# Performance work log

Hardware: AMD Instinct MI355X
Metric: run time of the kernel (lower is better)

Reference implementation:

```python
import jax, jax.numpy as jnp
import numpy as np

K = 3
IN_C, OUT_C = 64, 64
B, N, E = 2, 50000, 800000


def setup_inputs() -> dict:
    key = jax.random.key(0)
    k1, k2, k3, k4, k5 = jax.random.split(key, 5)
    x = jax.random.normal(k1, (B, N, IN_C), dtype=jnp.float32)
    edge_index = jax.random.randint(k2, (2, E), 0, N, dtype=jnp.int64)
    edge_weight = jax.random.uniform(k3, (E,), dtype=jnp.float32)
    stdv = 1.0 / np.sqrt(IN_C * K)
    weight = jax.random.uniform(k4, (K, IN_C, OUT_C), dtype=jnp.float32, minval=-stdv, maxval=stdv)
    bias = jax.random.uniform(k5, (OUT_C,), dtype=jnp.float32, minval=-stdv, maxval=stdv)
    return {"x": x, "edge_index": edge_index, "edge_weight": edge_weight, "weight": weight, "bias": bias}


def reference(x, edge_index, edge_weight, weight, bias):
    row, col = edge_index[0], edge_index[1]
    num_nodes = x.shape[1]
    # remove self loops (mask them out; equivalent math)
    keep = (row != col)
    ew = jnp.where(keep, edge_weight, 0.0)
    # degree counts edges per source node (ones), excluding self loops
    deg = jax.ops.segment_sum(keep.astype(x.dtype), row, num_segments=num_nodes)
    deg_inv_sqrt = jnp.where(deg > 0, deg ** -0.5, 0.0)
    lap = -deg_inv_sqrt[row] * ew * deg_inv_sqrt[col]  # [E]

    def spmm(m):
        # m: [B, N, C] -> gather cols, scale by lap, scatter-add to rows
        vals = m[:, col, :] * lap[None, :, None]        # [B, E, C]
        return jnp.zeros_like(m).at[:, row, :].add(vals)

    Tx0 = x
    out = jnp.matmul(Tx0, weight[0])
    Tx1 = spmm(Tx0)
    out = out + jnp.matmul(Tx1, weight[1])
    for k in range(2, weight.shape[0]):
        Tx2 = 2.0 * spmm(Tx1) - Tx0
        out = out + jnp.matmul(Tx2, weight[k])
        Tx0, Tx1 = Tx1, Tx2
    return out + bias
```

## Files before the change

kernel.cpp:

```cpp
#include <hip/hip_runtime.h>

#define N_NODES 50000
#define N_EDGES 800000
#define N_B 2
#define N_C 64
#define BN_ROWS (N_B * N_NODES)

__device__ inline unsigned short f2bf(float f) {
  unsigned int u = __float_as_uint(f);
  return (unsigned short)((u + 0x7fffu + ((u >> 16) & 1u)) >> 16);
}
__device__ inline float bf2f(unsigned short h) { return __uint_as_float(((unsigned int)h) << 16); }
__device__ inline float lof(unsigned int u) { return __uint_as_float(u << 16); }
__device__ inline float hif(unsigned int u) { return __uint_as_float(u & 0xffff0000u); }

__global__ __launch_bounds__(256) void k_deg(const int* __restrict__ ei, int* __restrict__ deg) {
  int e = blockIdx.x * 256 + threadIdx.x;
  if (e >= N_EDGES) return;
  int r = ei[e];
  int c = ei[N_EDGES + e];
  if (r != c) atomicAdd(&deg[r], 1);
}

__global__ __launch_bounds__(256) void k_offsets(const int* __restrict__ deg, int* __restrict__ counter,
                                                 int* __restrict__ rowptr, int* __restrict__ cursor,
                                                 float* __restrict__ dis) {
  int n = blockIdx.x * 256 + threadIdx.x;
  int lane = threadIdx.x & 63;
  int d = (n < N_NODES) ? deg[n] : 0;
  int pre = d;
#pragma unroll
  for (int off = 1; off < 64; off <<= 1) {
    int v = __shfl_up(pre, off);
    if (lane >= off) pre += v;
  }
  int waveTotal = __shfl(pre, 63);
  int wbase = 0;
  if (lane == 63) wbase = atomicAdd(counter, waveTotal);
  wbase = __shfl(wbase, 63);
  if (n < N_NODES) {
    int off0 = wbase + pre - d;
    rowptr[n] = off0;
    cursor[n] = off0;
    dis[n] = d > 0 ? rsqrtf((float)d) : 0.0f;
  }
}

__global__ __launch_bounds__(256) void k_fill(const int* __restrict__ ei, const float* __restrict__ ew,
                                              const float* __restrict__ dis, int* __restrict__ cursor,
                                              int2* __restrict__ ccv) {
  int e = blockIdx.x * 256 + threadIdx.x;
  if (e >= N_EDGES) return;
  int r = ei[e];
  int c = ei[N_EDGES + e];
  if (r == c) return;
  float v = -dis[r] * ew[e] * dis[c];
  int pos = atomicAdd(&cursor[r], 1);
  ccv[pos] = make_int2(c, __float_as_int(v));
}

__global__ __launch_bounds__(256) void k_cvt(const float* __restrict__ x, unsigned short* __restrict__ xb) {
  int i = blockIdx.x * 256 + threadIdx.x;
  if (i >= BN_ROWS * 16) return;
  float4 v = ((const float4*)x)[i];
  ushort4 h;
  h.x = f2bf(v.x); h.y = f2bf(v.y); h.z = f2bf(v.z); h.w = f2bf(v.w);
  ((ushort4*)xb)[i] = h;
}

#define UNPK_FMA(Q, A0, A1, A2, A3, A4, A5, A6, A7, V) \
  A0 += (V) * lof(Q.x); A1 += (V) * hif(Q.x); \
  A2 += (V) * lof(Q.y); A3 += (V) * hif(Q.y); \
  A4 += (V) * lof(Q.z); A5 += (V) * hif(Q.z); \
  A6 += (V) * lof(Q.w); A7 += (V) * hif(Q.w);

#define RED3(A) { A += __shfl_xor(A, 8); A += __shfl_xor(A, 16); A += __shfl_xor(A, 32); }

template <int BFOUT>
__global__ __launch_bounds__(256) void k_spmm(const unsigned short* __restrict__ src, void* __restrict__ dstv,
                                              const int* __restrict__ rowptr, const int* __restrict__ deg,
                                              const int2* __restrict__ ccv) {
  int n = (blockIdx.x * 256 + threadIdx.x) >> 6;
  int lane = threadIdx.x & 63;
  if (n >= N_NODES) return;
  const int g = lane >> 3;
  const int cg = lane & 7;
  const unsigned short* s0 = src;
  const unsigned short* s1 = src + (size_t)N_NODES * N_C;
  int r0 = rowptr[n];
  int end = r0 + deg[n];
  float a00 = 0, a01 = 0, a02 = 0, a03 = 0, a04 = 0, a05 = 0, a06 = 0, a07 = 0;
  float a10 = 0, a11 = 0, a12 = 0, a13 = 0, a14 = 0, a15 = 0, a16 = 0, a17 = 0;
#pragma unroll 2
  for (int i = r0; i < end; i += 8) {
    int idx = i + g;
    bool ok = idx < end;
    int2 pe = ccv[ok ? idx : (end - 1)];
    float val = ok ? __int_as_float(pe.y) : 0.0f;
    size_t off = (size_t)pe.x * N_C + cg * 8;
    uint4 q0 = *(const uint4*)(s0 + off);
    uint4 q1 = *(const uint4*)(s1 + off);
    UNPK_FMA(q0, a00, a01, a02, a03, a04, a05, a06, a07, val)
    UNPK_FMA(q1, a10, a11, a12, a13, a14, a15, a16, a17, val)
  }
  RED3(a00) RED3(a01) RED3(a02) RED3(a03) RED3(a04) RED3(a05) RED3(a06) RED3(a07)
  RED3(a10) RED3(a11) RED3(a12) RED3(a13) RED3(a14) RED3(a15) RED3(a16) RED3(a17)
  if (BFOUT) {
    unsigned short* d = (unsigned short*)dstv;
    if (g == 0) {
      uint4 o;
      o.x = (unsigned)f2bf(a00) | ((unsigned)f2bf(a01) << 16);
      o.y = (unsigned)f2bf(a02) | ((unsigned)f2bf(a03) << 16);
      o.z = (unsigned)f2bf(a04) | ((unsigned)f2bf(a05) << 16);
      o.w = (unsigned)f2bf(a06) | ((unsigned)f2bf(a07) << 16);
      *(uint4*)(d + (size_t)n * N_C + cg * 8) = o;
    } else if (g == 1) {
      uint4 o;
      o.x = (unsigned)f2bf(a10) | ((unsigned)f2bf(a11) << 16);
      o.y = (unsigned)f2bf(a12) | ((unsigned)f2bf(a13) << 16);
      o.z = (unsigned)f2bf(a14) | ((unsigned)f2bf(a15) << 16);
      o.w = (unsigned)f2bf(a16) | ((unsigned)f2bf(a17) << 16);
      *(uint4*)(d + ((size_t)N_NODES + n) * N_C + cg * 8) = o;
    }
  } else {
    float* d = (float*)dstv;
    if (g == 0) {
      *(float4*)(d + (size_t)n * N_C + cg * 8) = make_float4(a00, a01, a02, a03);
      *(float4*)(d + (size_t)n * N_C + cg * 8 + 4) = make_float4(a04, a05, a06, a07);
    } else if (g == 1) {
      *(float4*)(d + ((size_t)N_NODES + n) * N_C + cg * 8) = make_float4(a10, a11, a12, a13);
      *(float4*)(d + ((size_t)N_NODES + n) * N_C + cg * 8 + 4) = make_float4(a14, a15, a16, a17);
    }
  }
}

#define FMA4(ACC, AV, WV) \
  ACC.x += (AV) * (WV).x; ACC.y += (AV) * (WV).y; ACC.z += (AV) * (WV).z; ACC.w += (AV) * (WV).w;

#define CH_STEP(Wb, KK, A0, A1, A2, A3) { \
  const float4 wv0 = *(const float4*)&(Wb)[(k4 + (KK)) * 64 + tx8]; \
  const float4 wv1 = *(const float4*)&(Wb)[(k4 + (KK)) * 64 + tx8 + 4]; \
  FMA4(acc00, A0, wv0) FMA4(acc01, A0, wv1) \
  FMA4(acc10, A1, wv0) FMA4(acc11, A1, wv1) \
  FMA4(acc20, A2, wv0) FMA4(acc21, A2, wv1) \
  FMA4(acc30, A3, wv0) FMA4(acc31, A3, wv1) }

#define CH_BODY(A0, A1, A2, A3, Wb) \
    CH_STEP(Wb, 0, A0.x, A1.x, A2.x, A3.x) \
    CH_STEP(Wb, 1, A0.y, A1.y, A2.y, A3.y) \
    CH_STEP(Wb, 2, A0.z, A1.z, A2.z, A3.z) \
    CH_STEP(Wb, 3, A0.w, A1.w, A2.w, A3.w)

#define CH_PASS_F32(Ab, Wb) \
  _Pragma("unroll 2") \
  for (int k4 = 0; k4 < 64; k4 += 4) { \
    const float4 a0 = *(const float4*)&(Ab)[r0 * 64 + (size_t)k4]; \
    const float4 a1 = *(const float4*)&(Ab)[r1 * 64 + (size_t)k4]; \
    const float4 a2 = *(const float4*)&(Ab)[r2 * 64 + (size_t)k4]; \
    const float4 a3 = *(const float4*)&(Ab)[r3 * 64 + (size_t)k4]; \
    CH_BODY(a0, a1, a2, a3, Wb) \
  }

__device__ inline float4 u4f(ushort4 u) {
  return make_float4(bf2f(u.x), bf2f(u.y), bf2f(u.z), bf2f(u.w));
}

#define CH_PASS_BF(Ab, Wb) \
  _Pragma("unroll 2") \
  for (int k4 = 0; k4 < 64; k4 += 4) { \
    const float4 a0 = u4f(*(const ushort4*)&(Ab)[r0 * 64 + (size_t)k4]); \
    const float4 a1 = u4f(*(const ushort4*)&(Ab)[r1 * 64 + (size_t)k4]); \
    const float4 a2 = u4f(*(const ushort4*)&(Ab)[r2 * 64 + (size_t)k4]); \
    const float4 a3 = u4f(*(const ushort4*)&(Ab)[r3 * 64 + (size_t)k4]); \
    CH_BODY(a0, a1, a2, a3, Wb) \
  }

__global__ __launch_bounds__(256) void k_gemm(const unsigned short* __restrict__ xb,
                                              const unsigned short* __restrict__ t1h,
                                              const float* __restrict__ w,
                                              const float* __restrict__ bias,
                                              float* out) {
  __shared__ float wl[3 * 4096];
  int t = threadIdx.x;
  for (int i = t; i < 4096; i += 256) {
    float w0 = w[i];
    float w1 = w[4096 + i];
    float w2 = w[8192 + i];
    wl[i] = w0 - w2;
    wl[4096 + i] = w1;
    wl[8192 + i] = 2.0f * w2;
  }
  __syncthreads();
  const int tx8 = (t & 7) * 8;
  const int rg = t >> 3;
  const size_t base = (size_t)blockIdx.x * 128 + (size_t)rg * 4;
  const size_t rmax = BN_ROWS - 1;
  const size_t r0 = base + 0 < rmax ? base + 0 : rmax;
  const size_t r1 = base + 1 < rmax ? base + 1 : rmax;
  const size_t r2 = base + 2 < rmax ? base + 2 : rmax;
  const size_t r3 = base + 3 < rmax ? base + 3 : rmax;
  const float4 bv0 = *(const float4*)&bias[tx8];
  const float4 bv1 = *(const float4*)&bias[tx8 + 4];
  float4 acc00 = bv0, acc01 = bv1;
  float4 acc10 = bv0, acc11 = bv1;
  float4 acc20 = bv0, acc21 = bv1;
  float4 acc30 = bv0, acc31 = bv1;

  CH_PASS_BF(xb, wl)
  CH_PASS_BF(t1h, (wl + 4096))
  CH_PASS_F32(out, (wl + 8192))

  if (base + 0 < BN_ROWS) { *(float4*)&out[(base + 0) * 64 + tx8] = acc00; *(float4*)&out[(base + 0) * 64 + tx8 + 4] = acc01; }
  if (base + 1 < BN_ROWS) { *(float4*)&out[(base + 1) * 64 + tx8] = acc10; *(float4*)&out[(base + 1) * 64 + tx8 + 4] = acc11; }
  if (base + 2 < BN_ROWS) { *(float4*)&out[(base + 2) * 64 + tx8] = acc20; *(float4*)&out[(base + 2) * 64 + tx8 + 4] = acc21; }
  if (base + 3 < BN_ROWS) { *(float4*)&out[(base + 3) * 64 + tx8] = acc30; *(float4*)&out[(base + 3) * 64 + tx8 + 4] = acc31; }
}

extern "C" void kernel_launch(void* const* d_in, const int* in_sizes, int n_in,
                              void* d_out, int out_size, void* d_ws, size_t ws_size,
                              hipStream_t stream) {
  const float* x = (const float*)d_in[0];
  const int* ei = (const int*)d_in[1];
  const float* ew = (const float*)d_in[2];
  const float* w = (const float*)d_in[3];
  const float* bias = (const float*)d_in[4];
  float* out = (float*)d_out;

  int* ws32 = (int*)d_ws;
  const size_t NA = 50048;
  int* deg = ws32;
  int* counter = deg + N_NODES;
  int* cursor = ws32 + NA;
  float* dis = (float*)(cursor + NA);
  int* rowptr = (int*)(dis + NA);
  int2* ccv = (int2*)(rowptr + NA);
  unsigned short* xb = (unsigned short*)(rowptr + NA + 2 * N_EDGES);
  unsigned short* t1h = xb + (size_t)BN_ROWS * N_C;
  const size_t NEED = ((size_t)(4 * NA + 2 * N_EDGES) + (size_t)BN_ROWS * N_C) * 4;
  if (ws_size < NEED) return;

  hipMemsetAsync(deg, 0, (N_NODES + 1) * sizeof(int), stream);
  k_cvt<<<(BN_ROWS * 16 + 255) / 256, 256, 0, stream>>>(x, xb);
  k_deg<<<(N_EDGES + 255) / 256, 256, 0, stream>>>(ei, deg);
  k_offsets<<<(N_NODES + 255) / 256, 256, 0, stream>>>(deg, counter, rowptr, cursor, dis);
  k_fill<<<(N_EDGES + 255) / 256, 256, 0, stream>>>(ei, ew, dis, cursor, ccv);
  k_spmm<1><<<(N_NODES * 64 + 255) / 256, 256, 0, stream>>>(xb, t1h, rowptr, deg, ccv);
  k_spmm<0><<<(N_NODES * 64 + 255) / 256, 256, 0, stream>>>(t1h, out, rowptr, deg, ccv);
  k_gemm<<<(BN_ROWS + 127) / 128, 256, 0, stream>>>(xb, t1h, w, bias, out);
}
```

Baseline: 284.9 us.

## Restructure final GEMM with bf16 weights in LDS and two rows per thread

The final dense GEMM now stores its three combined weight matrices as bf16 in shared memory, which halves LDS footprint and read bandwidth. The three passes over x, T1 and the spmm output are fused into one k-loop with 16-byte vector loads. Each thread now handles two rows instead of four, so the grid doubles in size. The costs are extra unpack ALU work, bf16 rounding of the weights (lower precision), and weight LDS reads that are now amortized over two rows instead of four.

```diff
diff --git a/kernel.cpp b/kernel.cpp
--- a/kernel.cpp
+++ b/kernel.cpp
@@ -13,6 +13,20 @@
 __device__ inline float bf2f(unsigned short h) { return __uint_as_float(((unsigned int)h) << 16); }
 __device__ inline float lof(unsigned int u) { return __uint_as_float(u << 16); }
 __device__ inline float hif(unsigned int u) { return __uint_as_float(u & 0xffff0000u); }
+
+__device__ inline float bsel(uint4 q, int kk) {
+  unsigned int w = (kk < 2) ? q.x : (kk < 4) ? q.y : (kk < 6) ? q.z : q.w;
+  return (kk & 1) ? hif(w) : lof(w);
+}
+__device__ inline float fsel(float4 a, float4 b, int kk) {
+  float4 s = (kk < 4) ? a : b;
+  int m = kk & 3;
+  return m == 0 ? s.x : m == 1 ? s.y : m == 2 ? s.z : s.w;
+}
+__device__ inline void unpk8(uint4 q, float* f) {
+  f[0] = lof(q.x); f[1] = hif(q.x); f[2] = lof(q.y); f[3] = hif(q.y);
+  f[4] = lof(q.z); f[5] = hif(q.z); f[6] = lof(q.w); f[7] = hif(q.w);
+}
 
 __global__ __launch_bounds__(256) void k_deg(const int* __restrict__ ei, int* __restrict__ deg) {
   int e = blockIdx.x * 256 + threadIdx.x;
@@ -134,86 +148,88 @@
   }
 }
 
-#define FMA4(ACC, AV, WV) \
-  ACC.x += (AV) * (WV).x; ACC.y += (AV) * (WV).y; ACC.z += (AV) * (WV).z; ACC.w += (AV) * (WV).w;
-
-#define CH_STEP(Wb, KK, A0, A1, A2, A3) { \
-  const float4 wv0 = *(const float4*)&(Wb)[(k4 + (KK)) * 64 + tx8]; \
-  const float4 wv1 = *(const float4*)&(Wb)[(k4 + (KK)) * 64 + tx8 + 4]; \
-  FMA4(acc00, A0, wv0) FMA4(acc01, A0, wv1) \
-  FMA4(acc10, A1, wv0) FMA4(acc11, A1, wv1) \
-  FMA4(acc20, A2, wv0) FMA4(acc21, A2, wv1) \
-  FMA4(acc30, A3, wv0) FMA4(acc31, A3, wv1) }
-
-#define CH_BODY(A0, A1, A2, A3, Wb) \
-    CH_STEP(Wb, 0, A0.x, A1.x, A2.x, A3.x) \
-    CH_STEP(Wb, 1, A0.y, A1.y, A2.y, A3.y) \
-    CH_STEP(Wb, 2, A0.z, A1.z, A2.z, A3.z) \
-    CH_STEP(Wb, 3, A0.w, A1.w, A2.w, A3.w)
-
-#define CH_PASS_F32(Ab, Wb) \
-  _Pragma("unroll 2") \
-  for (int k4 = 0; k4 < 64; k4 += 4) { \
-    const float4 a0 = *(const float4*)&(Ab)[r0 * 64 + (size_t)k4]; \
-    const float4 a1 = *(const float4*)&(Ab)[r1 * 64 + (size_t)k4]; \
-    const float4 a2 = *(const float4*)&(Ab)[r2 * 64 + (size_t)k4]; \
-    const float4 a3 = *(const float4*)&(Ab)[r3 * 64 + (size_t)k4]; \
-    CH_BODY(a0, a1, a2, a3, Wb) \
-  }
-
-__device__ inline float4 u4f(ushort4 u) {
-  return make_float4(bf2f(u.x), bf2f(u.y), bf2f(u.z), bf2f(u.w));
-}
-
-#define CH_PASS_BF(Ab, Wb) \
-  _Pragma("unroll 2") \
-  for (int k4 = 0; k4 < 64; k4 += 4) { \
-    const float4 a0 = u4f(*(const ushort4*)&(Ab)[r0 * 64 + (size_t)k4]); \
-    const float4 a1 = u4f(*(const ushort4*)&(Ab)[r1 * 64 + (size_t)k4]); \
-    const float4 a2 = u4f(*(const ushort4*)&(Ab)[r2 * 64 + (size_t)k4]); \
-    const float4 a3 = u4f(*(const ushort4*)&(Ab)[r3 * 64 + (size_t)k4]); \
-    CH_BODY(a0, a1, a2, a3, Wb) \
-  }
-
 __global__ __launch_bounds__(256) void k_gemm(const unsigned short* __restrict__ xb,
                                               const unsigned short* __restrict__ t1h,
                                               const float* __restrict__ w,
                                               const float* __restrict__ bias,
                                               float* out) {
-  __shared__ float wl[3 * 4096];
+  __shared__ unsigned short wl[3 * 4096];
   int t = threadIdx.x;
   for (int i = t; i < 4096; i += 256) {
     float w0 = w[i];
     float w1 = w[4096 + i];
     float w2 = w[8192 + i];
-    wl[i] = w0 - w2;
-    wl[4096 + i] = w1;
-    wl[8192 + i] = 2.0f * w2;
+    wl[i] = f2bf(w0 - w2);
+    wl[4096 + i] = f2bf(w1);
+    wl[8192 + i] = f2bf(2.0f * w2);
   }
   __syncthreads();
   const int tx8 = (t & 7) * 8;
   const int rg = t >> 3;
-  const size_t base = (size_t)blockIdx.x * 128 + (size_t)rg * 4;
+  const size_t base = (size_t)blockIdx.x * 64 + (size_t)rg * 2;
   const size_t rmax = BN_ROWS - 1;
-  const size_t r0 = base + 0 < rmax ? base + 0 : rmax;
+  const size_t r0 = base < rmax ? base : rmax;
   const size_t r1 = base + 1 < rmax ? base + 1 : rmax;
-  const size_t r2 = base + 2 < rmax ? base + 2 : rmax;
-  const size_t r3 = base + 3 < rmax ? base + 3 : rmax;
-  const float4 bv0 = *(const float4*)&bias[tx8];
-  const float4 bv1 = *(const float4*)&bias[tx8 + 4];
-  float4 acc00 = bv0, acc01 = bv1;
-  float4 acc10 = bv0, acc11 = bv1;
-  float4 acc20 = bv0, acc21 = bv1;
-  float4 acc30 = bv0, acc31 = bv1;
-
-  CH_PASS_BF(xb, wl)
-  CH_PASS_BF(t1h, (wl + 4096))
-  CH_PASS_F32(out, (wl + 8192))
-
-  if (base + 0 < BN_ROWS) { *(float4*)&out[(base + 0) * 64 + tx8] = acc00; *(float4*)&out[(base + 0) * 64 + tx8 + 4] = acc01; }
-  if (base + 1 < BN_ROWS) { *(float4*)&out[(base + 1) * 64 + tx8] = acc10; *(float4*)&out[(base + 1) * 64 + tx8 + 4] = acc11; }
-  if (base + 2 < BN_ROWS) { *(float4*)&out[(base + 2) * 64 + tx8] = acc20; *(float4*)&out[(base + 2) * 64 + tx8 + 4] = acc21; }
-  if (base + 3 < BN_ROWS) { *(float4*)&out[(base + 3) * 64 + tx8] = acc30; *(float4*)&out[(base + 3) * 64 + tx8 + 4] = acc31; }
+  const unsigned short* xp0 = xb + r0 * 64;
+  const unsigned short* xp1 = xb + r1 * 64;
+  const unsigned short* tp0 = t1h + r0 * 64;
+  const unsigned short* tp1 = t1h + r1 * 64;
+  const float* zp0 = out + r0 * 64;
+  const float* zp1 = out + r1 * 64;
+
+  float a0[8], a1[8];
+  {
+    const float4 b0 = *(const float4*)&bias[tx8];
+    const float4 b1 = *(const float4*)&bias[tx8 + 4];
+    a0[0] = b0.x; a0[1] = b0.y; a0[2] = b0.z; a0[3] = b0.w;
+    a0[4] = b1.x; a0[5] = b1.y; a0[6] = b1.z; a0[7] = b1.w;
+#pragma unroll
+    for (int j = 0; j < 8; ++j) a1[j] = a0[j];
+  }
+
+#pragma unroll 2
+  for (int k8 = 0; k8 < 64; k8 += 8) {
+    uint4 x0q = *(const uint4*)(xp0 + k8);
+    uint4 x1q = *(const uint4*)(xp1 + k8);
+    uint4 t0q = *(const uint4*)(tp0 + k8);
+    uint4 t1q = *(const uint4*)(tp1 + k8);
+    float4 z00 = *(const float4*)(zp0 + k8);
+    float4 z01 = *(const float4*)(zp0 + k8 + 4);
+    float4 z10 = *(const float4*)(zp1 + k8);
+    float4 z11 = *(const float4*)(zp1 + k8 + 4);
+#pragma unroll
+    for (int kk = 0; kk < 8; ++kk) {
+      const int k = k8 + kk;
+      uint4 wq0 = *(const uint4*)&wl[k * 64 + tx8];
+      uint4 wq1 = *(const uint4*)&wl[4096 + k * 64 + tx8];
+      uint4 wq2 = *(const uint4*)&wl[8192 + k * 64 + tx8];
+      float wf0[8], wf1[8], wf2[8];
+      unpk8(wq0, wf0);
+      unpk8(wq1, wf1);
+      unpk8(wq2, wf2);
+      const float xv0 = bsel(x0q, kk), xv1 = bsel(x1q, kk);
+      const float tv0 = bsel(t0q, kk), tv1 = bsel(t1q, kk);
+      const float zv0 = fsel(z00, z01, kk), zv1 = fsel(z10, z11, kk);
+#pragma unroll
+      for (int j = 0; j < 8; ++j) {
+        a0[j] += xv0 * wf0[j];
+        a1[j] += xv1 * wf0[j];
+        a0[j] += tv0 * wf1[j];
+        a1[j] += tv1 * wf1[j];
+        a0[j] += zv0 * wf2[j];
+        a1[j] += zv1 * wf2[j];
+      }
+    }
+  }
+
+  if (base < BN_ROWS) {
+    *(float4*)&out[base * 64 + tx8] = make_float4(a0[0], a0[1], a0[2], a0[3]);
+    *(float4*)&out[base * 64 + tx8 + 4] = make_float4(a0[4], a0[5], a0[6], a0[7]);
+  }
+  if (base + 1 < BN_ROWS) {
+    *(float4*)&out[(base + 1) * 64 + tx8] = make_float4(a1[0], a1[1], a1[2], a1[3]);
+    *(float4*)&out[(base + 1) * 64 + tx8 + 4] = make_float4(a1[4], a1[5], a1[6], a1[7]);
+  }
 }
 
 extern "C" void kernel_launch(void* const* d_in, const int* in_sizes, int n_in,
@@ -246,5 +262,5 @@
   k_fill<<<(N_EDGES + 255) / 256, 256, 0, stream>>>(ei, ew, dis, cursor, ccv);
   k_spmm<1><<<(N_NODES * 64 + 255) / 256, 256, 0, stream>>>(xb, t1h, rowptr, deg, ccv);
   k_spmm<0><<<(N_NODES * 64 + 255) / 256, 256, 0, stream>>>(t1h, out, rowptr, deg, ccv);
-  k_gemm<<<(BN_ROWS + 127) / 128, 256, 0, stream>>>(xb, t1h, w, bias, out);
-}
+  k_gemm<<<(BN_ROWS + 63) / 64, 256, 0, stream>>>(xb, t1h, w, bias, out);
+}
```

Result: slower. 309.3 us (+8.5%).

## Replace scalar FMA dense projection with bf16 MFMA 16x16x32 kernel

Applied to the files above, without the earlier changes.

Rewrites the final combined GEMM (x, Tx1, spmm(Tx1) against the folded Chebyshev weights) to use bf16 MFMA instructions. Weights are pre-packed into LDS in bf16 fragment layout, and each wave computes a 16-row by 64-column tile from register-loaded A fragments. The fp32 spmm output is rounded to bf16 before multiplying, which lowers precision. The intent is to remove the scalar FMA compute cost of the projection stage, which is only one of several kernels in the pipeline.

```diff
diff --git a/kernel.cpp b/kernel.cpp
--- a/kernel.cpp
+++ b/kernel.cpp
@@ -5,6 +5,9 @@
 #define N_B 2
 #define N_C 64
 #define BN_ROWS (N_B * N_NODES)
+
+typedef __attribute__((ext_vector_type(8))) short short8;
+typedef __attribute__((ext_vector_type(4))) float f32x4;
 
 __device__ inline unsigned short f2bf(float f) {
   unsigned int u = __float_as_uint(f);
@@ -134,86 +137,89 @@
   }
 }
 
-#define FMA4(ACC, AV, WV) \
-  ACC.x += (AV) * (WV).x; ACC.y += (AV) * (WV).y; ACC.z += (AV) * (WV).z; ACC.w += (AV) * (WV).w;
-
-#define CH_STEP(Wb, KK, A0, A1, A2, A3) { \
-  const float4 wv0 = *(const float4*)&(Wb)[(k4 + (KK)) * 64 + tx8]; \
-  const float4 wv1 = *(const float4*)&(Wb)[(k4 + (KK)) * 64 + tx8 + 4]; \
-  FMA4(acc00, A0, wv0) FMA4(acc01, A0, wv1) \
-  FMA4(acc10, A1, wv0) FMA4(acc11, A1, wv1) \
-  FMA4(acc20, A2, wv0) FMA4(acc21, A2, wv1) \
-  FMA4(acc30, A3, wv0) FMA4(acc31, A3, wv1) }
-
-#define CH_BODY(A0, A1, A2, A3, Wb) \
-    CH_STEP(Wb, 0, A0.x, A1.x, A2.x, A3.x) \
-    CH_STEP(Wb, 1, A0.y, A1.y, A2.y, A3.y) \
-    CH_STEP(Wb, 2, A0.z, A1.z, A2.z, A3.z) \
-    CH_STEP(Wb, 3, A0.w, A1.w, A2.w, A3.w)
-
-#define CH_PASS_F32(Ab, Wb) \
-  _Pragma("unroll 2") \
-  for (int k4 = 0; k4 < 64; k4 += 4) { \
-    const float4 a0 = *(const float4*)&(Ab)[r0 * 64 + (size_t)k4]; \
-    const float4 a1 = *(const float4*)&(Ab)[r1 * 64 + (size_t)k4]; \
-    const float4 a2 = *(const float4*)&(Ab)[r2 * 64 + (size_t)k4]; \
-    const float4 a3 = *(const float4*)&(Ab)[r3 * 64 + (size_t)k4]; \
-    CH_BODY(a0, a1, a2, a3, Wb) \
-  }
-
-__device__ inline float4 u4f(ushort4 u) {
-  return make_float4(bf2f(u.x), bf2f(u.y), bf2f(u.z), bf2f(u.w));
-}
-
-#define CH_PASS_BF(Ab, Wb) \
-  _Pragma("unroll 2") \
-  for (int k4 = 0; k4 < 64; k4 += 4) { \
-    const float4 a0 = u4f(*(const ushort4*)&(Ab)[r0 * 64 + (size_t)k4]); \
-    const float4 a1 = u4f(*(const ushort4*)&(Ab)[r1 * 64 + (size_t)k4]); \
-    const float4 a2 = u4f(*(const ushort4*)&(Ab)[r2 * 64 + (size_t)k4]); \
-    const float4 a3 = u4f(*(const ushort4*)&(Ab)[r3 * 64 + (size_t)k4]); \
-    CH_BODY(a0, a1, a2, a3, Wb) \
-  }
-
 __global__ __launch_bounds__(256) void k_gemm(const unsigned short* __restrict__ xb,
                                               const unsigned short* __restrict__ t1h,
                                               const float* __restrict__ w,
                                               const float* __restrict__ bias,
                                               float* out) {
-  __shared__ float wl[3 * 4096];
-  int t = threadIdx.x;
-  for (int i = t; i < 4096; i += 256) {
-    float w0 = w[i];
-    float w1 = w[4096 + i];
-    float w2 = w[8192 + i];
-    wl[i] = w0 - w2;
-    wl[4096 + i] = w1;
-    wl[8192 + i] = 2.0f * w2;
+  __shared__ unsigned short bp[6 * 4 * 64 * 8];
+  const int t = threadIdx.x;
+  for (int idx = t; idx < 1536; idx += 256) {
+    int kt = idx >> 8;
+    int rem = idx & 255;
+    int c = rem >> 6;
+    int l = rem & 63;
+    int ch = kt >> 1;
+    int kbase = (kt & 1) * 32 + (l >> 4) * 8;
+    int n = c * 16 + (l & 15);
+    unsigned short* dst = &bp[idx * 8];
+#pragma unroll
+    for (int j = 0; j < 8; ++j) {
+      int k = kbase + j;
+      float v;
+      if (ch == 0)      v = w[k * 64 + n] - w[8192 + k * 64 + n];
+      else if (ch == 1) v = w[4096 + k * 64 + n];
+      else              v = 2.0f * w[8192 + k * 64 + n];
+      dst[j] = f2bf(v);
+    }
   }
   __syncthreads();
-  const int tx8 = (t & 7) * 8;
-  const int rg = t >> 3;
-  const size_t base = (size_t)blockIdx.x * 128 + (size_t)rg * 4;
-  const size_t rmax = BN_ROWS - 1;
-  const size_t r0 = base + 0 < rmax ? base + 0 : rmax;
-  const size_t r1 = base + 1 < rmax ? base + 1 : rmax;
-  const size_t r2 = base + 2 < rmax ? base + 2 : rmax;
-  const size_t r3 = base + 3 < rmax ? base + 3 : rmax;
-  const float4 bv0 = *(const float4*)&bias[tx8];
-  const float4 bv1 = *(const float4*)&bias[tx8 + 4];
-  float4 acc00 = bv0, acc01 = bv1;
-  float4 acc10 = bv0, acc11 = bv1;
-  float4 acc20 = bv0, acc21 = bv1;
-  float4 acc30 = bv0, acc31 = bv1;
-
-  CH_PASS_BF(xb, wl)
-  CH_PASS_BF(t1h, (wl + 4096))
-  CH_PASS_F32(out, (wl + 8192))
-
-  if (base + 0 < BN_ROWS) { *(float4*)&out[(base + 0) * 64 + tx8] = acc00; *(float4*)&out[(base + 0) * 64 + tx8 + 4] = acc01; }
-  if (base + 1 < BN_ROWS) { *(float4*)&out[(base + 1) * 64 + tx8] = acc10; *(float4*)&out[(base + 1) * 64 + tx8 + 4] = acc11; }
-  if (base + 2 < BN_ROWS) { *(float4*)&out[(base + 2) * 64 + tx8] = acc20; *(float4*)&out[(base + 2) * 64 + tx8 + 4] = acc21; }
-  if (base + 3 < BN_ROWS) { *(float4*)&out[(base + 3) * 64 + tx8] = acc30; *(float4*)&out[(base + 3) * 64 + tx8 + 4] = acc31; }
+
+  const int wid = t >> 6;
+  const int lane = t & 63;
+  const size_t base = (size_t)blockIdx.x * 64 + (size_t)wid * 16;
+  const int arow = lane & 15;
+  const int ko = (lane >> 4) * 8;
+  size_t row = base + arow;
+  if (row > (size_t)(BN_ROWS - 1)) row = BN_ROWS - 1;
+
+  const unsigned short* xp = xb + row * 64 + ko;
+  const unsigned short* tp = t1h + row * 64 + ko;
+  const float* zp = out + row * 64 + ko;
+  short8 ax0 = *(const short8*)(xp);
+  short8 ax1 = *(const short8*)(xp + 32);
+  short8 at0 = *(const short8*)(tp);
+  short8 at1 = *(const short8*)(tp + 32);
+  float4 z00 = *(const float4*)(zp);
+  float4 z01 = *(const float4*)(zp + 4);
+  float4 z10 = *(const float4*)(zp + 32);
+  float4 z11 = *(const float4*)(zp + 36);
+  short8 az0, az1;
+  az0[0] = (short)f2bf(z00.x); az0[1] = (short)f2bf(z00.y);
+  az0[2] = (short)f2bf(z00.z); az0[3] = (short)f2bf(z00.w);
+  az0[4] = (short)f2bf(z01.x); az0[5] = (short)f2bf(z01.y);
+  az0[6] = (short)f2bf(z01.z); az0[7] = (short)f2bf(z01.w);
+  az1[0] = (short)f2bf(z10.x); az1[1] = (short)f2bf(z10.y);
+  az1[2] = (short)f2bf(z10.z); az1[3] = (short)f2bf(z10.w);
+  az1[4] = (short)f2bf(z11.x); az1[5] = (short)f2bf(z11.y);
+  az1[6] = (short)f2bf(z11.z); az1[7] = (short)f2bf(z11.w);
+
+  const int col = lane & 15;
+  const int rgrp = lane >> 4;
+
+#pragma unroll
+  for (int c = 0; c < 4; ++c) {
+    const unsigned short* bb = &bp[(size_t)c * 64 * 8];
+    short8 b0 = *(const short8*)(bb + (0 * 4 * 64 + lane) * 8);
+    short8 b1 = *(const short8*)(bb + (1 * 4 * 64 + lane) * 8);
+    short8 b2 = *(const short8*)(bb + (2 * 4 * 64 + lane) * 8);
+    short8 b3 = *(const short8*)(bb + (3 * 4 * 64 + lane) * 8);
+    short8 b4 = *(const short8*)(bb + (4 * 4 * 64 + lane) * 8);
+    short8 b5 = *(const short8*)(bb + (5 * 4 * 64 + lane) * 8);
+    f32x4 acc = {0.f, 0.f, 0.f, 0.f};
+    acc = __builtin_amdgcn_mfma_f32_16x16x32_bf16(ax0, b0, acc, 0, 0, 0);
+    acc = __builtin_amdgcn_mfma_f32_16x16x32_bf16(ax1, b1, acc, 0, 0, 0);
+    acc = __builtin_amdgcn_mfma_f32_16x16x32_bf16(at0, b2, acc, 0, 0, 0);
+    acc = __builtin_amdgcn_mfma_f32_16x16x32_bf16(at1, b3, acc, 0, 0, 0);
+    acc = __builtin_amdgcn_mfma_f32_16x16x32_bf16(az0, b4, acc, 0, 0, 0);
+    acc = __builtin_amdgcn_mfma_f32_16x16x32_bf16(az1, b5, acc, 0, 0, 0);
+    const float bcol = bias[c * 16 + col];
+#pragma unroll
+    for (int j = 0; j < 4; ++j) {
+      size_t r = base + (size_t)(rgrp * 4 + j);
+      if (r < BN_ROWS) out[r * 64 + c * 16 + col] = acc[j] + bcol;
+    }
+  }
 }
 
 extern "C" void kernel_launch(void* const* d_in, const int* in_sizes, int n_in,
@@ -246,5 +252,5 @@
   k_fill<<<(N_EDGES + 255) / 256, 256, 0, stream>>>(ei, ew, dis, cursor, ccv);
   k_spmm<1><<<(N_NODES * 64 + 255) / 256, 256, 0, stream>>>(xb, t1h, rowptr, deg, ccv);
   k_spmm<0><<<(N_NODES * 64 + 255) / 256, 256, 0, stream>>>(t1h, out, rowptr, deg, ccv);
-  k_gemm<<<(BN_ROWS + 127) / 128, 256, 0, stream>>>(xb, t1h, w, bias, out);
-}
+  k_gemm<<<(BN_ROWS + 63) / 64, 256, 0, stream>>>(xb, t1h, w, bias, out);
+}
```

Result: faster. 279.3 us (-2.0%).
